# Performance work log

Measured on AMD Instinct MI355X. Metric: run time of the kernel, lower is better.

The kernel has to match this reference:

```python
import jax, jax.numpy as jnp
import numpy as np

B, T, D = 8, 2048, 1024
GAMMA = 0.96875


def setup_inputs() -> dict:
    key = jax.random.key(0)
    ks = jax.random.split(key, 7)
    sD = 1.0 / np.sqrt(D)
    sT = 1.0 / np.sqrt(T)
    return {
        "x": jax.random.normal(ks[0], (B, T, D), dtype=jnp.float32),
        "Wq": jax.random.normal(ks[1], (D, D), dtype=jnp.float32) * sD,
        "Wk": jax.random.normal(ks[2], (D, D), dtype=jnp.float32) * sD,
        "Wv": jax.random.normal(ks[3], (D, D), dtype=jnp.float32) * sD,
        "W_ih": jax.random.normal(ks[4], (T, T), dtype=jnp.float32) * sT,
        "W_hh": jax.random.normal(ks[5], (T, T), dtype=jnp.float32) * sT,
        "b_ih": jax.random.normal(ks[6], (T,), dtype=jnp.float32) * sT,
    }


def reference(x, Wq, Wk, Wv, W_ih, W_hh, b_ih):
    # x: [B, T, D]; QKV projections (Linear with no bias: x @ W^T)
    Q = jnp.einsum("btd,ed->bte", x, Wq)
    K = jnp.einsum("btd,ed->bte", x, Wk)
    V = jnp.einsum("btd,ed->bte", x, Wv)

    # retention state injected as hidden bias of the tanh-RNN: [B, T]
    bias = jnp.sum(K * V, axis=-1)

    gamma = jnp.full((T,), GAMMA, dtype=x.dtype)
    u = gamma @ W_ih.T + b_ih  # input contribution, identical every step: [T]

    def step(h, b_t):
        h_new = jnp.tanh(u + h @ W_hh.T + b_t)
        return h_new, h_new

    h0 = jnp.zeros((T,), dtype=x.dtype)
    _, S = jax.lax.scan(step, h0, bias)  # scan over the B rows -> S: [B, T]

    # vmap(mul)(S, Q^T)^T  ==  out[b,t,d] = S[b,t] * Q[b,t,d]
    return S[:, :, None] * Q
```

## Files before the change

### kernel.cpp

```cpp
#include <hip/hip_runtime.h>
#include <stdint.h>

#define T_DIM 2048
#define D_DIM 1024
#define B_DIM 8
#define M_TOK (B_DIM * T_DIM)
#define GAMMA_C 0.96875f

typedef float f32x4 __attribute__((ext_vector_type(4)));
typedef float f32x16 __attribute__((ext_vector_type(16)));
typedef float fl4 __attribute__((ext_vector_type(4)));
typedef __bf16 bf16x8 __attribute__((ext_vector_type(8)));
typedef unsigned short us8 __attribute__((ext_vector_type(8)));
typedef unsigned short us4 __attribute__((ext_vector_type(4)));

__device__ __forceinline__ unsigned short f32_bf16_rne(float f) {
  uint32_t u = __builtin_bit_cast(uint32_t, f);
  return (unsigned short)((u + 0x7FFFu + ((u >> 16) & 1u)) >> 16);
}
__device__ __forceinline__ float bf16_f32(unsigned short h) {
  uint32_t u = ((uint32_t)h) << 16;
  return __builtin_bit_cast(float, u);
}

__device__ __forceinline__ int swz_row(int r) {
  return ((r >> 1) & 3) ^ ((r >> 3) & 3);
}

__device__ __forceinline__ void gload16(const void* g, void* l) {
  __builtin_amdgcn_global_load_lds(
      reinterpret_cast<const __attribute__((address_space(1))) uint32_t*>(
          reinterpret_cast<uintptr_t>(g)),
      reinterpret_cast<__attribute__((address_space(3))) uint32_t*>(
          reinterpret_cast<uintptr_t>(l)),
      16, 0, 0);
}

__device__ __forceinline__ bf16x8 ldfrag(const unsigned short* p) {
  us8 u = *reinterpret_cast<const us8*>(p);
  return __builtin_bit_cast(bf16x8, u);
}

__global__ __launch_bounds__(256) void k_split(const float* __restrict__ in, int n8,
                                               unsigned short* __restrict__ hi,
                                               unsigned short* __restrict__ lo) {
  int stride = gridDim.x * blockDim.x;
  for (int i = blockIdx.x * blockDim.x + threadIdx.x; i < n8; i += stride) {
    fl4 v0 = ((const fl4*)in)[i * 2];
    fl4 v1 = ((const fl4*)in)[i * 2 + 1];
    us8 h, l;
#pragma unroll
    for (int j = 0; j < 4; ++j) {
      unsigned short hb = f32_bf16_rne(v0[j]);
      h[j] = hb;
      l[j] = f32_bf16_rne(v0[j] - bf16_f32(hb));
      unsigned short hb1 = f32_bf16_rne(v1[j]);
      h[j + 4] = hb1;
      l[j + 4] = f32_bf16_rne(v1[j] - bf16_f32(hb1));
    }
    ((us8*)hi)[i] = h;
    ((us8*)lo)[i] = l;
  }
}

__global__ __launch_bounds__(256) void k_split_hi(const float* __restrict__ in, int n8,
                                                  unsigned short* __restrict__ hi) {
  int stride = gridDim.x * blockDim.x;
  for (int i = blockIdx.x * blockDim.x + threadIdx.x; i < n8; i += stride) {
    fl4 v0 = ((const fl4*)in)[i * 2];
    fl4 v1 = ((const fl4*)in)[i * 2 + 1];
    us8 h;
#pragma unroll
    for (int j = 0; j < 4; ++j) {
      h[j] = f32_bf16_rne(v0[j]);
      h[j + 4] = f32_bf16_rne(v1[j]);
    }
    ((us8*)hi)[i] = h;
  }
}

__global__ __launch_bounds__(256) void k_split_T(const float* __restrict__ in,
                                                 unsigned short* __restrict__ th,
                                                 unsigned short* __restrict__ tl) {
  __shared__ float tile[64][69];
  int be = blockIdx.x >> 4, bd = blockIdx.x & 15;
  int e0 = be * 64, d0 = bd * 64;
  int r = threadIdx.x >> 4;
  int c = (threadIdx.x & 15) * 4;
#pragma unroll
  for (int it = 0; it < 4; ++it) {
    int rr = r + it * 16;
    fl4 v = *(const fl4*)(in + (size_t)(e0 + rr) * D_DIM + d0 + c);
#pragma unroll
    for (int j = 0; j < 4; ++j) tile[rr][c + j] = v[j];
  }
  __syncthreads();
#pragma unroll
  for (int it = 0; it < 4; ++it) {
    int dr = r + it * 16;
    us4 h, l;
#pragma unroll
    for (int j = 0; j < 4; ++j) {
      float f = tile[c + j][dr];
      h[j] = f32_bf16_rne(f);
      l[j] = f32_bf16_rne(f - bf16_f32(h[j]));
    }
    *(us4*)(th + (size_t)(d0 + dr) * D_DIM + e0 + c) = h;
    *(us4*)(tl + (size_t)(d0 + dr) * D_DIM + e0 + c) = l;
  }
}

__global__ __launch_bounds__(256) void k_u(const float* __restrict__ Wih,
                                           const float* __restrict__ bih,
                                           float* __restrict__ u) {
  int wave = threadIdx.x >> 6, lane = threadIdx.x & 63;
  int t = blockIdx.x * 4 + wave;
  const fl4* row = (const fl4*)(Wih + (size_t)t * T_DIM);
  float s = 0.f;
#pragma unroll
  for (int i = 0; i < 8; ++i) {
    fl4 v = row[lane + i * 64];
    s += v[0] + v[1] + v[2] + v[3];
  }
#pragma unroll
  for (int m = 32; m >= 1; m >>= 1) s += __shfl_xor(s, m, 64);
  if (lane == 0) u[t] = GAMMA_C * s + bih[t];
}

__global__ __launch_bounds__(256) void k_step_bf(const unsigned short* __restrict__ Whh_b,
                                                 const float* __restrict__ hprev,
                                                 const float* __restrict__ u,
                                                 const float* __restrict__ biasrow,
                                                 float* __restrict__ hout) {
  int wave = threadIdx.x >> 6, lane = threadIdx.x & 63;
  int t = blockIdx.x * 4 + wave;
  const unsigned short* row = Whh_b + (size_t)t * T_DIM;
  float s = 0.f;
#pragma unroll
  for (int i = 0; i < 4; ++i) {
    us8 w = *(const us8*)(row + i * 512 + lane * 8);
    fl4 h0 = *(const fl4*)(hprev + i * 512 + lane * 8);
    fl4 h1 = *(const fl4*)(hprev + i * 512 + lane * 8 + 4);
    s += bf16_f32(w[0]) * h0[0] + bf16_f32(w[1]) * h0[1] +
         bf16_f32(w[2]) * h0[2] + bf16_f32(w[3]) * h0[3] +
         bf16_f32(w[4]) * h1[0] + bf16_f32(w[5]) * h1[1] +
         bf16_f32(w[6]) * h1[2] + bf16_f32(w[7]) * h1[3];
  }
#pragma unroll
  for (int m = 32; m >= 1; m >>= 1) s += __shfl_xor(s, m, 64);
  if (lane == 0) hout[t] = tanhf(u[t] + s + biasrow[t]);
}

__device__ __forceinline__ void map_blk(int bid, int& mb, int& nb) {
  int sw = (bid & 7) * 128 + (bid >> 3);
  mb = sw >> 3;
  nb = sw & 7;
}

__global__ __launch_bounds__(256) void k_ht(
    const unsigned short* __restrict__ ah, const unsigned short* __restrict__ al,
    const unsigned short* __restrict__ bh, const unsigned short* __restrict__ bl,
    float* __restrict__ Hf) {
  __shared__ unsigned short sAh[2][64 * 32], sAl[2][64 * 32];
  __shared__ unsigned short sBh[2][64 * 32], sBl[2][64 * 32];
  const int tid = threadIdx.x;
  const int wave = tid >> 6, lane = tid & 63;
  const int wm = wave >> 1, wn = wave & 1;
  const int m0 = (blockIdx.x >> 4) * 64, n0 = (blockIdx.x & 15) * 64;
  const int hi32 = lane >> 5;

  const int srow = tid >> 2;
  const int csrc = (tid & 3) ^ swz_row(srow);
  const size_t ga = (size_t)(m0 + srow) * D_DIM + csrc * 8;
  const size_t gb = (size_t)(n0 + srow) * D_DIM + csrc * 8;
  const int ldst = tid * 8;

  f32x16 acc = {};
  const int l31 = lane & 31;
  const int sw = swz_row(l31);
  const int ar = wm * 32 + l31;
  const int br = wn * 32 + l31;
  int aoff[2], boff[2];
#pragma unroll
  for (int kh = 0; kh < 2; ++kh) {
    aoff[kh] = ar * 32 + (((kh * 2 + hi32) ^ sw) * 8);
    boff[kh] = br * 32 + (((kh * 2 + hi32) ^ sw) * 8);
  }

#define HT_STAGE(t, buf)                         \
  do {                                           \
    const size_t ko = (size_t)(t) * 32;          \
    gload16(ah + ga + ko, &sAh[buf][ldst]);      \
    gload16(al + ga + ko, &sAl[buf][ldst]);      \
    gload16(bh + gb + ko, &sBh[buf][ldst]);      \
    gload16(bl + gb + ko, &sBl[buf][ldst]);      \
  } while (0)

  HT_STAGE(0, 0);
  __syncthreads();
  for (int kt = 0; kt < 32; ++kt) {
    const int cur = kt & 1;
    if (kt < 31) HT_STAGE(kt + 1, cur ^ 1);
#pragma unroll
    for (int kh = 0; kh < 2; ++kh) {
      bf16x8 fah = ldfrag(&sAh[cur][aoff[kh]]);
      bf16x8 fal = ldfrag(&sAl[cur][aoff[kh]]);
      bf16x8 fbh = ldfrag(&sBh[cur][boff[kh]]);
      bf16x8 fbl = ldfrag(&sBl[cur][boff[kh]]);
      acc = __builtin_amdgcn_mfma_f32_32x32x16_bf16(fah, fbh, acc, 0, 0, 0);
      acc = __builtin_amdgcn_mfma_f32_32x32x16_bf16(fah, fbl, acc, 0, 0, 0);
      acc = __builtin_amdgcn_mfma_f32_32x32x16_bf16(fal, fbh, acc, 0, 0, 0);
    }
    __syncthreads();
  }
#pragma unroll
  for (int r = 0; r < 16; ++r) {
    int row = m0 + wm * 32 + (r & 3) + 8 * (r >> 2) + 4 * hi32;
    int col = n0 + wn * 32 + l31;
    Hf[(size_t)row * D_DIM + col] = acc[r];
  }
#undef HT_STAGE
}

__global__ __launch_bounds__(256) void k_nprime(const float* __restrict__ Hf,
                                                unsigned short* __restrict__ mh,
                                                unsigned short* __restrict__ ml) {
  __shared__ float t2[64][65];
  const int ti = blockIdx.x >> 4;
  const int tj = blockIdx.x & 15;
  const int r0 = ti * 64, c0 = tj * 64;
  const int a = threadIdx.x >> 2;
  const int b4 = (threadIdx.x & 3) * 16;
  if (tj < ti) {
#pragma unroll
    for (int j = 0; j < 16; ++j) {
      size_t ad = (size_t)(r0 + a) * D_DIM + c0 + b4 + j;
      mh[ad] = 0;
      ml[ad] = 0;
    }
    return;
  }
#pragma unroll
  for (int j = 0; j < 16; j += 4) {
    fl4 v = *(const fl4*)(Hf + (size_t)(c0 + a) * D_DIM + r0 + b4 + j);
#pragma unroll
    for (int q = 0; q < 4; ++q) t2[a][b4 + j + q] = v[q];
  }
  __syncthreads();
#pragma unroll
  for (int j = 0; j < 16; ++j) {
    int dp = r0 + a;
    int dd = c0 + b4 + j;
    float v = 0.f;
    if (dd > dp)       v = Hf[(size_t)dp * D_DIM + dd] + t2[b4 + j][a];
    else if (dd == dp) v = Hf[(size_t)dp * D_DIM + dd];
    unsigned short hb = f32_bf16_rne(v);
    unsigned short lb = f32_bf16_rne(v - bf16_f32(hb));
    size_t ad = (size_t)dp * D_DIM + dd;
    mh[ad] = hb;
    ml[ad] = lb;
  }
}

__global__ __launch_bounds__(256, 2) void k_y_bias(
    const unsigned short* __restrict__ xh, const unsigned short* __restrict__ xl,
    const unsigned short* __restrict__ bh, const unsigned short* __restrict__ bl,
    const float* __restrict__ xf, float* __restrict__ bias) {
  __shared__ unsigned short sAh[2][128 * 32], sAl[2][128 * 32];
  __shared__ unsigned short sBh[2][128 * 32], sBl[2][128 * 32];
  const int tid = threadIdx.x;
  const int wave = tid >> 6, lane = tid & 63;
  const int wm = wave >> 1, wn = wave & 1;
  int mb, nb;
  map_blk(blockIdx.x, mb, nb);
  const int m0 = mb * 128, n0 = nb * 128;
  const int hi32 = lane >> 5;
  const int kt0 = nb * 4;

  const int srow0 = tid >> 2, srow1 = srow0 + 64;
  const int csrc0 = (tid & 3) ^ swz_row(srow0);
  const int csrc1 = (tid & 3) ^ swz_row(srow1);
  const size_t gaA0 = (size_t)(m0 + srow0) * D_DIM + csrc0 * 8;
  const size_t gaA1 = (size_t)(m0 + srow1) * D_DIM + csrc1 * 8;
  const size_t gaB0 = (size_t)(n0 + srow0) * D_DIM + csrc0 * 8;
  const size_t gaB1 = (size_t)(n0 + srow1) * D_DIM + csrc1 * 8;
  const int ldst0 = tid * 8, ldst1 = (tid + 256) * 8;

  f32x16 acc[2][2] = {};
  const int l31 = lane & 31;
  const int sw = swz_row(l31);
  int aoff[2][2], boff[2][2];
#pragma unroll
  for (int mi = 0; mi < 2; ++mi) {
    int r = wm * 64 + mi * 32 + l31;
#pragma unroll
    for (int kh = 0; kh < 2; ++kh)
      aoff[mi][kh] = r * 32 + (((kh * 2 + hi32) ^ sw) * 8);
  }
#pragma unroll
  for (int ni = 0; ni < 2; ++ni) {
    int r = wn * 64 + ni * 32 + l31;
#pragma unroll
    for (int kh = 0; kh < 2; ++kh)
      boff[ni][kh] = r * 32 + (((kh * 2 + hi32) ^ sw) * 8);
  }

#define Y_STAGE(t, buf)                           \
  do {                                            \
    const size_t ko = (size_t)(t) * 32;           \
    gload16(xh + gaA0 + ko, &sAh[buf][ldst0]);    \
    gload16(xh + gaA1 + ko, &sAh[buf][ldst1]);    \
    gload16(xl + gaA0 + ko, &sAl[buf][ldst0]);    \
    gload16(xl + gaA1 + ko, &sAl[buf][ldst1]);    \
    gload16(bh + gaB0 + ko, &sBh[buf][ldst0]);    \
    gload16(bh + gaB1 + ko, &sBh[buf][ldst1]);    \
    gload16(bl + gaB0 + ko, &sBl[buf][ldst0]);    \
    gload16(bl + gaB1 + ko, &sBl[buf][ldst1]);    \
  } while (0)

  Y_STAGE(kt0, 0);
  __syncthreads();
  for (int kt = kt0; kt < 32; ++kt) {
    const int cur = (kt - kt0) & 1;
    if (kt < 31) Y_STAGE(kt + 1, cur ^ 1);
#pragma unroll
    for (int kh = 0; kh < 2; ++kh) {
      bf16x8 fah[2], fal[2], fbh_[2], fbl_[2];
#pragma unroll
      for (int mi = 0; mi < 2; ++mi) {
        fah[mi] = ldfrag(&sAh[cur][aoff[mi][kh]]);
        fal[mi] = ldfrag(&sAl[cur][aoff[mi][kh]]);
      }
#pragma unroll
      for (int ni = 0; ni < 2; ++ni) {
        fbh_[ni] = ldfrag(&sBh[cur][boff[ni][kh]]);
        fbl_[ni] = ldfrag(&sBl[cur][boff[ni][kh]]);
      }
      __builtin_amdgcn_s_setprio(1);
#pragma unroll
      for (int mi = 0; mi < 2; ++mi)
#pragma unroll
        for (int ni = 0; ni < 2; ++ni) {
          acc[mi][ni] = __builtin_amdgcn_mfma_f32_32x32x16_bf16(fah[mi], fbh_[ni], acc[mi][ni], 0, 0, 0);
          acc[mi][ni] = __builtin_amdgcn_mfma_f32_32x32x16_bf16(fah[mi], fbl_[ni], acc[mi][ni], 0, 0, 0);
          acc[mi][ni] = __builtin_amdgcn_mfma_f32_32x32x16_bf16(fal[mi], fbh_[ni], acc[mi][ni], 0, 0, 0);
        }
      __builtin_amdgcn_s_setprio(0);
    }
    __syncthreads();
  }

#pragma unroll
  for (int mi = 0; mi < 2; ++mi)
#pragma unroll
    for (int r = 0; r < 16; ++r) {
      int row = m0 + wm * 64 + mi * 32 + (r & 3) + 8 * (r >> 2) + 4 * hi32;
      const float* xr = xf + (size_t)row * D_DIM + n0 + wn * 64 + l31;
      float p = xr[0] * acc[mi][0][r] + xr[32] * acc[mi][1][r];
      p += __shfl_xor(p, 1, 64);
      p += __shfl_xor(p, 2, 64);
      p += __shfl_xor(p, 4, 64);
      p += __shfl_xor(p, 8, 64);
      p += __shfl_xor(p, 16, 64);
      if (l31 == 0) atomicAdd(&bias[row], p);
    }
#undef Y_STAGE
}

__global__ __launch_bounds__(256, 4) void k_q_out(
    const unsigned short* __restrict__ xh,
    const unsigned short* __restrict__ qh_,
    const float* __restrict__ S, float* __restrict__ out) {
  __shared__ unsigned short sA[2][128 * 32];
  __shared__ unsigned short sB[2][128 * 32];
  const int tid = threadIdx.x;
  const int wave = tid >> 6, lane = tid & 63;
  const int wm = wave >> 1, wn = wave & 1;
  int mb, nb;
  map_blk(blockIdx.x, mb, nb);
  const int m0 = mb * 128, n0 = nb * 128;
  const int hi32 = lane >> 5;

  const int srow0 = tid >> 2, srow1 = srow0 + 64;
  const int csrc0 = (tid & 3) ^ swz_row(srow0);
  const int csrc1 = (tid & 3) ^ swz_row(srow1);
  const size_t gaA0 = (size_t)(m0 + srow0) * D_DIM + csrc0 * 8;
  const size_t gaA1 = (size_t)(m0 + srow1) * D_DIM + csrc1 * 8;
  const size_t gaB0 = (size_t)(n0 + srow0) * D_DIM + csrc0 * 8;
  const size_t gaB1 = (size_t)(n0 + srow1) * D_DIM + csrc1 * 8;
  const int ldst0 = tid * 8, ldst1 = (tid + 256) * 8;

  f32x16 acc[2][2] = {};
  const int l31 = lane & 31;
  const int sw = swz_row(l31);
  int aoff[2][2], boff[2][2];
#pragma unroll
  for (int mi = 0; mi < 2; ++mi) {
    int r = wm * 64 + mi * 32 + l31;
#pragma unroll
    for (int kh = 0; kh < 2; ++kh)
      aoff[mi][kh] = r * 32 + (((kh * 2 + hi32) ^ sw) * 8);
  }
#pragma unroll
  for (int ni = 0; ni < 2; ++ni) {
    int r = wn * 64 + ni * 32 + l31;
#pragma unroll
    for (int kh = 0; kh < 2; ++kh)
      boff[ni][kh] = r * 32 + (((kh * 2 + hi32) ^ sw) * 8);
  }

#define Q_STAGE(t, buf)                           \
  do {                                            \
    const size_t ko = (size_t)(t) * 32;           \
    gload16(xh + gaA0 + ko, &sA[buf][ldst0]);     \
    gload16(xh + gaA1 + ko, &sA[buf][ldst1]);     \
    gload16(qh_ + gaB0 + ko, &sB[buf][ldst0]);    \
    gload16(qh_ + gaB1 + ko, &sB[buf][ldst1]);    \
  } while (0)

  Q_STAGE(0, 0);
  __syncthreads();
  for (int kt = 0; kt < 32; ++kt) {
    const int cur = kt & 1;
    if (kt < 31) Q_STAGE(kt + 1, cur ^ 1);
#pragma unroll
    for (int kh = 0; kh < 2; ++kh) {
      bf16x8 fa[2], fb[2];
#pragma unroll
      for (int mi = 0; mi < 2; ++mi) fa[mi] = ldfrag(&sA[cur][aoff[mi][kh]]);
#pragma unroll
      for (int ni = 0; ni < 2; ++ni) fb[ni] = ldfrag(&sB[cur][boff[ni][kh]]);
      __builtin_amdgcn_s_setprio(1);
#pragma unroll
      for (int mi = 0; mi < 2; ++mi)
#pragma unroll
        for (int ni = 0; ni < 2; ++ni)
          acc[mi][ni] = __builtin_amdgcn_mfma_f32_32x32x16_bf16(fa[mi], fb[ni], acc[mi][ni], 0, 0, 0);
      __builtin_amdgcn_s_setprio(0);
    }
    __syncthreads();
  }

#pragma unroll
  for (int mi = 0; mi < 2; ++mi)
#pragma unroll
    for (int r = 0; r < 16; ++r) {
      int row = m0 + wm * 64 + mi * 32 + (r & 3) + 8 * (r >> 2) + 4 * hi32;
      float sc = S[row];
      float* orow = out + (size_t)row * D_DIM + n0 + wn * 64 + l31;
      orow[0] = sc * acc[mi][0][r];
      orow[32] = sc * acc[mi][1][r];
    }
#undef Q_STAGE
}

extern "C" void kernel_launch(void* const* d_in, const int* in_sizes, int n_in,
                              void* d_out, int out_size, void* d_ws, size_t ws_size,
                              hipStream_t stream) {
  const float* x   = (const float*)d_in[0];
  const float* Wq  = (const float*)d_in[1];
  const float* Wk  = (const float*)d_in[2];
  const float* Wv  = (const float*)d_in[3];
  const float* Wih = (const float*)d_in[4];
  const float* Whh = (const float*)d_in[5];
  const float* bih = (const float*)d_in[6];
  float* out = (float*)d_out;

  char* ws = (char*)d_ws;
  size_t off = 0;
  auto alloc = [&](size_t bytes) -> char* {
    char* p = ws + off;
    off += (bytes + 255) & ~(size_t)255;
    return p;
  };
  unsigned short* xh   = (unsigned short*)alloc((size_t)M_TOK * D_DIM * 2);
  unsigned short* xl   = (unsigned short*)alloc((size_t)M_TOK * D_DIM * 2);
  unsigned short* wqh  = (unsigned short*)alloc((size_t)D_DIM * D_DIM * 2);
  unsigned short* wkth = (unsigned short*)alloc((size_t)D_DIM * D_DIM * 2);
  unsigned short* wktl = (unsigned short*)alloc((size_t)D_DIM * D_DIM * 2);
  unsigned short* wvth = (unsigned short*)alloc((size_t)D_DIM * D_DIM * 2);
  unsigned short* wvtl = (unsigned short*)alloc((size_t)D_DIM * D_DIM * 2);
  unsigned short* mph  = (unsigned short*)alloc((size_t)D_DIM * D_DIM * 2);
  unsigned short* mpl  = (unsigned short*)alloc((size_t)D_DIM * D_DIM * 2);
  float* Hf   = (float*)alloc((size_t)D_DIM * D_DIM * 4);
  float* bias = (float*)alloc((size_t)M_TOK * 4);
  float* Sbuf = (float*)alloc((size_t)M_TOK * 4);
  float* ubuf = (float*)alloc((size_t)T_DIM * 4);
  float* zbuf = (float*)alloc((size_t)T_DIM * 4);
  unsigned short* whhb = wkth;
  (void)ws_size; (void)in_sizes; (void)n_in; (void)out_size;

  k_split<<<2048, 256, 0, stream>>>(x, M_TOK * D_DIM / 8, xh, xl);
  k_split_hi<<<512, 256, 0, stream>>>(Wq, D_DIM * D_DIM / 8, wqh);
  k_split_T<<<256, 256, 0, stream>>>(Wk, wkth, wktl);
  k_split_T<<<256, 256, 0, stream>>>(Wv, wvth, wvtl);

  hipMemsetAsync(bias, 0, (size_t)M_TOK * 4, stream);
  hipMemsetAsync(zbuf, 0, (size_t)T_DIM * 4, stream);

  k_u<<<T_DIM / 4, 256, 0, stream>>>(Wih, bih, ubuf);

  k_ht<<<256, 256, 0, stream>>>(wvth, wvtl, wkth, wktl, Hf);

  k_nprime<<<256, 256, 0, stream>>>(Hf, mph, mpl);

  k_split_hi<<<1024, 256, 0, stream>>>(Whh, T_DIM * T_DIM / 8, whhb);

  k_y_bias<<<1024, 256, 0, stream>>>(xh, xl, mph, mpl, x, bias);

  for (int b = 0; b < B_DIM; ++b) {
    const float* hp = (b == 0) ? zbuf : (Sbuf + (size_t)(b - 1) * T_DIM);
    k_step_bf<<<T_DIM / 4, 256, 0, stream>>>(whhb, hp, ubuf, bias + (size_t)b * T_DIM,
                                             Sbuf + (size_t)b * T_DIM);
  }

  k_q_out<<<1024, 256, 0, stream>>>(xh, wqh, Sbuf, out);
}
```

Baseline: 261.7 us.

## Prefetch two stages ahead with vmcnt waits and pair triangular tiles in bias GEMM

The three MFMA GEMM kernels now issue loads two K-steps ahead and wait with explicit s_waitcnt vmcnt plus a raw barrier, instead of __syncthreads after issuing only the next stage. The goal is to hide global-to-LDS latency better. In k_y_bias each block now handles two column tiles (np and 7-np) of the triangular reduction, which evens out the work per block and halves the grid. Its epilogue also rebuilds x from the hi/lo bf16 pair rather than reading the fp32 x. The explicit vmcnt counts depend on exact load ordering, and the paired-tile scheme changes the mapping of blocks to XCDs.

```diff
diff --git a/kernel.cpp b/kernel.cpp
--- a/kernel.cpp
+++ b/kernel.cpp
@@ -39,6 +39,19 @@
 __device__ __forceinline__ bf16x8 ldfrag(const unsigned short* p) {
   us8 u = *reinterpret_cast<const us8*>(p);
   return __builtin_bit_cast(bf16x8, u);
+}
+
+__device__ __forceinline__ void wait_vm8_bar() {
+  asm volatile("s_waitcnt vmcnt(8)" ::: "memory");
+  __builtin_amdgcn_s_barrier();
+}
+__device__ __forceinline__ void wait_vm4_bar() {
+  asm volatile("s_waitcnt vmcnt(4)" ::: "memory");
+  __builtin_amdgcn_s_barrier();
+}
+__device__ __forceinline__ void wait_vm0_bar() {
+  asm volatile("s_waitcnt vmcnt(0)" ::: "memory");
+  __builtin_amdgcn_s_barrier();
 }
 
 __global__ __launch_bounds__(256) void k_split(const float* __restrict__ in, int n8,
@@ -149,12 +162,6 @@
 #pragma unroll
   for (int m = 32; m >= 1; m >>= 1) s += __shfl_xor(s, m, 64);
   if (lane == 0) hout[t] = tanhf(u[t] + s + biasrow[t]);
-}
-
-__device__ __forceinline__ void map_blk(int bid, int& mb, int& nb) {
-  int sw = (bid & 7) * 128 + (bid >> 3);
-  mb = sw >> 3;
-  nb = sw & 7;
 }
 
 __global__ __launch_bounds__(256) void k_ht(
@@ -187,20 +194,19 @@
     boff[kh] = br * 32 + (((kh * 2 + hi32) ^ sw) * 8);
   }
 
-#define HT_STAGE(t, buf)                         \
-  do {                                           \
-    const size_t ko = (size_t)(t) * 32;          \
-    gload16(ah + ga + ko, &sAh[buf][ldst]);      \
-    gload16(al + ga + ko, &sAl[buf][ldst]);      \
-    gload16(bh + gb + ko, &sBh[buf][ldst]);      \
-    gload16(bl + gb + ko, &sBl[buf][ldst]);      \
-  } while (0)
-
-  HT_STAGE(0, 0);
-  __syncthreads();
+  auto stage = [&](int t, int buf) {
+    const size_t ko = (size_t)t * 32;
+    gload16(ah + ga + ko, &sAh[buf][ldst]);
+    gload16(al + ga + ko, &sAl[buf][ldst]);
+    gload16(bh + gb + ko, &sBh[buf][ldst]);
+    gload16(bl + gb + ko, &sBl[buf][ldst]);
+  };
+
+  stage(0, 0);
+  stage(1, 1);
   for (int kt = 0; kt < 32; ++kt) {
     const int cur = kt & 1;
-    if (kt < 31) HT_STAGE(kt + 1, cur ^ 1);
+    if (kt < 31) wait_vm4_bar(); else wait_vm0_bar();
 #pragma unroll
     for (int kh = 0; kh < 2; ++kh) {
       bf16x8 fah = ldfrag(&sAh[cur][aoff[kh]]);
@@ -211,7 +217,8 @@
       acc = __builtin_amdgcn_mfma_f32_32x32x16_bf16(fah, fbl, acc, 0, 0, 0);
       acc = __builtin_amdgcn_mfma_f32_32x32x16_bf16(fal, fbh, acc, 0, 0, 0);
     }
-    __syncthreads();
+    __builtin_amdgcn_s_barrier();
+    if (kt + 2 <= 31) stage(kt + 2, cur);
   }
 #pragma unroll
   for (int r = 0; r < 16; ++r) {
@@ -219,7 +226,6 @@
     int col = n0 + wn * 32 + l31;
     Hf[(size_t)row * D_DIM + col] = acc[r];
   }
-#undef HT_STAGE
 }
 
 __global__ __launch_bounds__(256) void k_nprime(const float* __restrict__ Hf,
@@ -265,28 +271,25 @@
 __global__ __launch_bounds__(256, 2) void k_y_bias(
     const unsigned short* __restrict__ xh, const unsigned short* __restrict__ xl,
     const unsigned short* __restrict__ bh, const unsigned short* __restrict__ bl,
-    const float* __restrict__ xf, float* __restrict__ bias) {
+    float* __restrict__ bias) {
   __shared__ unsigned short sAh[2][128 * 32], sAl[2][128 * 32];
   __shared__ unsigned short sBh[2][128 * 32], sBl[2][128 * 32];
   const int tid = threadIdx.x;
   const int wave = tid >> 6, lane = tid & 63;
   const int wm = wave >> 1, wn = wave & 1;
-  int mb, nb;
-  map_blk(blockIdx.x, mb, nb);
-  const int m0 = mb * 128, n0 = nb * 128;
+  const int xcd = blockIdx.x & 7, seq = blockIdx.x >> 3;
+  const int mb = xcd * 16 + (seq >> 2);
+  const int np = seq & 3;
+  const int m0 = mb * 128;
   const int hi32 = lane >> 5;
-  const int kt0 = nb * 4;
 
   const int srow0 = tid >> 2, srow1 = srow0 + 64;
   const int csrc0 = (tid & 3) ^ swz_row(srow0);
   const int csrc1 = (tid & 3) ^ swz_row(srow1);
   const size_t gaA0 = (size_t)(m0 + srow0) * D_DIM + csrc0 * 8;
   const size_t gaA1 = (size_t)(m0 + srow1) * D_DIM + csrc1 * 8;
-  const size_t gaB0 = (size_t)(n0 + srow0) * D_DIM + csrc0 * 8;
-  const size_t gaB1 = (size_t)(n0 + srow1) * D_DIM + csrc1 * 8;
   const int ldst0 = tid * 8, ldst1 = (tid + 256) * 8;
 
-  f32x16 acc[2][2] = {};
   const int l31 = lane & 31;
   const int sw = swz_row(l31);
   int aoff[2][2], boff[2][2];
@@ -305,66 +308,78 @@
       boff[ni][kh] = r * 32 + (((kh * 2 + hi32) ^ sw) * 8);
   }
 
-#define Y_STAGE(t, buf)                           \
-  do {                                            \
-    const size_t ko = (size_t)(t) * 32;           \
-    gload16(xh + gaA0 + ko, &sAh[buf][ldst0]);    \
-    gload16(xh + gaA1 + ko, &sAh[buf][ldst1]);    \
-    gload16(xl + gaA0 + ko, &sAl[buf][ldst0]);    \
-    gload16(xl + gaA1 + ko, &sAl[buf][ldst1]);    \
-    gload16(bh + gaB0 + ko, &sBh[buf][ldst0]);    \
-    gload16(bh + gaB1 + ko, &sBh[buf][ldst1]);    \
-    gload16(bl + gaB0 + ko, &sBl[buf][ldst0]);    \
-    gload16(bl + gaB1 + ko, &sBl[buf][ldst1]);    \
-  } while (0)
-
-  Y_STAGE(kt0, 0);
-  __syncthreads();
-  for (int kt = kt0; kt < 32; ++kt) {
-    const int cur = (kt - kt0) & 1;
-    if (kt < 31) Y_STAGE(kt + 1, cur ^ 1);
-#pragma unroll
-    for (int kh = 0; kh < 2; ++kh) {
-      bf16x8 fah[2], fal[2], fbh_[2], fbl_[2];
-#pragma unroll
-      for (int mi = 0; mi < 2; ++mi) {
-        fah[mi] = ldfrag(&sAh[cur][aoff[mi][kh]]);
-        fal[mi] = ldfrag(&sAl[cur][aoff[mi][kh]]);
+  auto run_phase = [&](int nb) {
+    const int n0 = nb * 128;
+    const int kt0 = nb * 4;
+    const size_t gB0 = (size_t)(n0 + srow0) * D_DIM + csrc0 * 8;
+    const size_t gB1 = (size_t)(n0 + srow1) * D_DIM + csrc1 * 8;
+
+    auto stage = [&](int t, int buf) {
+      const size_t ko = (size_t)t * 32;
+      gload16(xh + gaA0 + ko, &sAh[buf][ldst0]);
+      gload16(xh + gaA1 + ko, &sAh[buf][ldst1]);
+      gload16(xl + gaA0 + ko, &sAl[buf][ldst0]);
+      gload16(xl + gaA1 + ko, &sAl[buf][ldst1]);
+      gload16(bh + gB0 + ko, &sBh[buf][ldst0]);
+      gload16(bh + gB1 + ko, &sBh[buf][ldst1]);
+      gload16(bl + gB0 + ko, &sBl[buf][ldst0]);
+      gload16(bl + gB1 + ko, &sBl[buf][ldst1]);
+    };
+
+    f32x16 acc[2][2] = {};
+    stage(kt0, 0);
+    stage(kt0 + 1, 1);
+    for (int kt = kt0; kt < 32; ++kt) {
+      const int cur = (kt - kt0) & 1;
+      if (kt < 31) wait_vm8_bar(); else wait_vm0_bar();
+#pragma unroll
+      for (int kh = 0; kh < 2; ++kh) {
+        bf16x8 fah[2], fal[2], fbh_[2], fbl_[2];
+#pragma unroll
+        for (int mi = 0; mi < 2; ++mi) {
+          fah[mi] = ldfrag(&sAh[cur][aoff[mi][kh]]);
+          fal[mi] = ldfrag(&sAl[cur][aoff[mi][kh]]);
+        }
+#pragma unroll
+        for (int ni = 0; ni < 2; ++ni) {
+          fbh_[ni] = ldfrag(&sBh[cur][boff[ni][kh]]);
+          fbl_[ni] = ldfrag(&sBl[cur][boff[ni][kh]]);
+        }
+        __builtin_amdgcn_s_setprio(1);
+#pragma unroll
+        for (int mi = 0; mi < 2; ++mi)
+#pragma unroll
+          for (int ni = 0; ni < 2; ++ni) {
+            acc[mi][ni] = __builtin_amdgcn_mfma_f32_32x32x16_bf16(fah[mi], fbh_[ni], acc[mi][ni], 0, 0, 0);
+            acc[mi][ni] = __builtin_amdgcn_mfma_f32_32x32x16_bf16(fah[mi], fbl_[ni], acc[mi][ni], 0, 0, 0);
+            acc[mi][ni] = __builtin_amdgcn_mfma_f32_32x32x16_bf16(fal[mi], fbh_[ni], acc[mi][ni], 0, 0, 0);
+          }
+        __builtin_amdgcn_s_setprio(0);
       }
-#pragma unroll
-      for (int ni = 0; ni < 2; ++ni) {
-        fbh_[ni] = ldfrag(&sBh[cur][boff[ni][kh]]);
-        fbl_[ni] = ldfrag(&sBl[cur][boff[ni][kh]]);
+      __builtin_amdgcn_s_barrier();
+      if (kt + 2 <= 31) stage(kt + 2, cur);
+    }
+
+#pragma unroll
+    for (int mi = 0; mi < 2; ++mi)
+#pragma unroll
+      for (int r = 0; r < 16; ++r) {
+        int row = m0 + wm * 64 + mi * 32 + (r & 3) + 8 * (r >> 2) + 4 * hi32;
+        size_t ix = (size_t)row * D_DIM + n0 + wn * 64 + l31;
+        float xv0 = bf16_f32(xh[ix]) + bf16_f32(xl[ix]);
+        float xv1 = bf16_f32(xh[ix + 32]) + bf16_f32(xl[ix + 32]);
+        float p = xv0 * acc[mi][0][r] + xv1 * acc[mi][1][r];
+        p += __shfl_xor(p, 1, 64);
+        p += __shfl_xor(p, 2, 64);
+        p += __shfl_xor(p, 4, 64);
+        p += __shfl_xor(p, 8, 64);
+        p += __shfl_xor(p, 16, 64);
+        if (l31 == 0) atomicAdd(&bias[row], p);
       }
-      __builtin_amdgcn_s_setprio(1);
-#pragma unroll
-      for (int mi = 0; mi < 2; ++mi)
-#pragma unroll
-        for (int ni = 0; ni < 2; ++ni) {
-          acc[mi][ni] = __builtin_amdgcn_mfma_f32_32x32x16_bf16(fah[mi], fbh_[ni], acc[mi][ni], 0, 0, 0);
-          acc[mi][ni] = __builtin_amdgcn_mfma_f32_32x32x16_bf16(fah[mi], fbl_[ni], acc[mi][ni], 0, 0, 0);
-          acc[mi][ni] = __builtin_amdgcn_mfma_f32_32x32x16_bf16(fal[mi], fbh_[ni], acc[mi][ni], 0, 0, 0);
-        }
-      __builtin_amdgcn_s_setprio(0);
-    }
-    __syncthreads();
-  }
-
-#pragma unroll
-  for (int mi = 0; mi < 2; ++mi)
-#pragma unroll
-    for (int r = 0; r < 16; ++r) {
-      int row = m0 + wm * 64 + mi * 32 + (r & 3) + 8 * (r >> 2) + 4 * hi32;
-      const float* xr = xf + (size_t)row * D_DIM + n0 + wn * 64 + l31;
-      float p = xr[0] * acc[mi][0][r] + xr[32] * acc[mi][1][r];
-      p += __shfl_xor(p, 1, 64);
-      p += __shfl_xor(p, 2, 64);
-      p += __shfl_xor(p, 4, 64);
-      p += __shfl_xor(p, 8, 64);
-      p += __shfl_xor(p, 16, 64);
-      if (l31 == 0) atomicAdd(&bias[row], p);
-    }
-#undef Y_STAGE
+  };
+
+  run_phase(np);
+  run_phase(7 - np);
 }
 
 __global__ __launch_bounds__(256, 4) void k_q_out(
@@ -376,8 +391,8 @@
   const int tid = threadIdx.x;
   const int wave = tid >> 6, lane = tid & 63;
   const int wm = wave >> 1, wn = wave & 1;
-  int mb, nb;
-  map_blk(blockIdx.x, mb, nb);
+  int sw0 = (blockIdx.x & 7) * 128 + (blockIdx.x >> 3);
+  const int mb = sw0 >> 3, nb = sw0 & 7;
   const int m0 = mb * 128, n0 = nb * 128;
   const int hi32 = lane >> 5;
 
@@ -409,20 +424,19 @@
       boff[ni][kh] = r * 32 + (((kh * 2 + hi32) ^ sw) * 8);
   }
 
-#define Q_STAGE(t, buf)                           \
-  do {                                            \
-    const size_t ko = (size_t)(t) * 32;           \
-    gload16(xh + gaA0 + ko, &sA[buf][ldst0]);     \
-    gload16(xh + gaA1 + ko, &sA[buf][ldst1]);     \
-    gload16(qh_ + gaB0 + ko, &sB[buf][ldst0]);    \
-    gload16(qh_ + gaB1 + ko, &sB[buf][ldst1]);    \
-  } while (0)
-
-  Q_STAGE(0, 0);
-  __syncthreads();
+  auto stage = [&](int t, int buf) {
+    const size_t ko = (size_t)t * 32;
+    gload16(xh + gaA0 + ko, &sA[buf][ldst0]);
+    gload16(xh + gaA1 + ko, &sA[buf][ldst1]);
+    gload16(qh_ + gaB0 + ko, &sB[buf][ldst0]);
+    gload16(qh_ + gaB1 + ko, &sB[buf][ldst1]);
+  };
+
+  stage(0, 0);
+  stage(1, 1);
   for (int kt = 0; kt < 32; ++kt) {
     const int cur = kt & 1;
-    if (kt < 31) Q_STAGE(kt + 1, cur ^ 1);
+    if (kt < 31) wait_vm4_bar(); else wait_vm0_bar();
 #pragma unroll
     for (int kh = 0; kh < 2; ++kh) {
       bf16x8 fa[2], fb[2];
@@ -438,7 +452,8 @@
           acc[mi][ni] = __builtin_amdgcn_mfma_f32_32x32x16_bf16(fa[mi], fb[ni], acc[mi][ni], 0, 0, 0);
       __builtin_amdgcn_s_setprio(0);
     }
-    __syncthreads();
+    __builtin_amdgcn_s_barrier();
+    if (kt + 2 <= 31) stage(kt + 2, cur);
   }
 
 #pragma unroll
@@ -451,7 +466,6 @@
       orow[0] = sc * acc[mi][0][r];
       orow[32] = sc * acc[mi][1][r];
     }
-#undef Q_STAGE
 }
 
 extern "C" void kernel_launch(void* const* d_in, const int* in_sizes, int n_in,
@@ -506,7 +520,7 @@
 
   k_split_hi<<<1024, 256, 0, stream>>>(Whh, T_DIM * T_DIM / 8, whhb);
 
-  k_y_bias<<<1024, 256, 0, stream>>>(xh, xl, mph, mpl, x, bias);
+  k_y_bias<<<512, 256, 0, stream>>>(xh, xl, mph, mpl, bias);
 
   for (int b = 0; b < B_DIM; ++b) {
     const float* hp = (b == 0) ? zbuf : (Sbuf + (size_t)(b - 1) * T_DIM);
```

Result: faster. 236.3 us (-9.7%).
